# Performance work log

Measured on AMD Instinct MI355X. Metric: run time of the kernel, lower is better.

The kernel has to match this reference:

```python
import jax, jax.numpy as jnp
import numpy as np

B, S = 512, 256
NUM_LOC, NUM_USERS, D = 50000, 10000, 256
MAX_RECENT = 5
DQ = D // 4            # user/hour/weekday embed dim
TEMP = 3 * DQ          # temporal feature size
H2 = D // 2            # scorer hidden
NEG = -1e9


def setup_inputs() -> dict:
    key = jax.random.key(0)
    ks = jax.random.split(key, 25)
    p = lambda i, shape: jax.random.normal(ks[i], shape, jnp.float32) * 0.02

    locations = jax.random.randint(ks[0], (B, S), 0, NUM_LOC)
    users = jax.random.randint(ks[1], (B, S), 0, NUM_USERS)
    weekdays = jax.random.randint(ks[2], (B, S), 0, 8)
    start_mins = jax.random.randint(ks[3], (B, S), 0, 1440)
    lengths = jax.random.randint(ks[4], (B,), 1, S + 1)  # ragged valid lengths
    mask = jnp.arange(S)[None, :] < lengths[:, None]     # (B,S) bool prefix mask

    return {
        "locations": locations, "users": users, "weekdays": weekdays,
        "start_mins": start_mins, "mask": mask,
        # embedding tables (padding_idx=0 row zeroed, matching torch init)
        "loc_table": p(5, (NUM_LOC, D)).at[0].set(0.0),
        "user_table": p(6, (NUM_USERS, DQ)).at[0].set(0.0),
        "hour_table": p(7, (25, DQ)).at[0].set(0.0),
        "wd_table": p(8, (8, DQ)).at[0].set(0.0),
        # LSTM (PyTorch layout: gates i,f,g,o stacked)
        "W_ih": p(9, (4 * D, D + TEMP)), "W_hh": p(10, (4 * D, D)),
        "b_ih": p(11, (4 * D,)), "b_hh": p(12, (4 * D,)),
        # recent-location scorer MLP
        "sc_W1": p(13, (H2, D + 2)), "sc_b1": p(14, (H2,)),
        "sc_W2": p(15, (1, H2)), "sc_b2": p(16, (1,)),
        # new-location predictor MLP (dropout is identity in eval)
        "np_W1": p(17, (D, D)), "np_b1": p(18, (D,)),
        "np_W2": p(19, (NUM_LOC, D)), "np_b2": p(20, (NUM_LOC,)),
        # mix predictor
        "mx_W": p(21, (1, D)), "mx_b": p(22, (1,)),
    }


def _forward(locations, users, weekdays, start_mins, mask,
             loc_table, user_table, hour_table, wd_table,
             W_ih, W_hh, b_ih, b_hh,
             sc_W1, sc_b1, sc_W2, sc_b2,
             np_W1, np_b1, np_W2, np_b2, mx_W, mx_b):
    gelu = lambda x: jax.nn.gelu(x, approximate=False)  # torch nn.GELU default

    hours = jnp.clip(start_mins // 60, 0, 24)
    temporal = jnp.concatenate(
        [user_table[users], hour_table[hours], wd_table[weekdays]], axis=-1)
    x = jnp.concatenate([loc_table[locations], temporal], axis=-1)  # (B,S,D+TEMP)

    # --- LSTM over time via scan (PyTorch gate order i,f,g,o) ---
    def step(carry, xt):
        h, c = carry
        g = xt @ W_ih.T + b_ih + h @ W_hh.T + b_hh
        i, f, gg, o = jnp.split(g, 4, axis=-1)
        c = jax.nn.sigmoid(f) * c + jax.nn.sigmoid(i) * jnp.tanh(gg)
        h = jax.nn.sigmoid(o) * jnp.tanh(c)
        return (h, c), h

    h0 = jnp.zeros((x.shape[0], D), x.dtype)
    _, outs = jax.lax.scan(step, (h0, h0), jnp.swapaxes(x, 0, 1))
    output = jnp.swapaxes(outs, 0, 1)  # (B,S,D)

    seq_lens = mask.sum(axis=1).astype(jnp.int32) - 1  # last valid index
    bids = jnp.arange(output.shape[0])
    context = output[bids, seq_lens]                   # (B,D)

    # --- vectorized ragged recent-location scoring (j=0 is last visit) ---
    j = jnp.arange(MAX_RECENT)
    idx = seq_lens[:, None] - j[None, :]               # (B,R) indices from end
    valid = idx >= 0                                   # j < seq_len_b
    idxc = jnp.clip(idx, 0, S - 1)
    bidx = bids[:, None]
    rlocs = locations[bidx, idxc]                      # (B,R)
    rtimes = start_mins[bidx, idxc]
    cur_time = start_mins[bids, seq_lens][:, None]
    tdiff = ((cur_time - rtimes).astype(jnp.float32) / 1440.0)[..., None]
    pos = jnp.broadcast_to(j.astype(jnp.float32), rlocs.shape)[..., None]
    feats = jnp.concatenate([loc_table[rlocs], tdiff, pos], axis=-1)  # (B,R,D+2)
    scores = (gelu(feats @ sc_W1.T + sc_b1) @ sc_W2.T + sc_b2)[..., 0]  # (B,R)

    # drop entry jj if some newer valid entry j' < jj has the same location.
    eq = rlocs[:, :, None] == rlocs[:, None, :]        # (B, jj, j')
    newer = (j[:, None] > j[None, :])[None]            # jj > j'
    dup = jnp.any(eq & newer & valid[:, None, :], axis=-1)
    keep = valid & ~dup
    scatter_locs = jnp.where(keep, rlocs, NUM_LOC)     # out-of-range -> dropped

    recent_logits = jnp.full((rlocs.shape[0], NUM_LOC), NEG, jnp.float32)
    recent_logits = recent_logits.at[bidx, scatter_locs].set(scores, mode='drop')

    new_logits = gelu(context @ np_W1.T + np_b1) @ np_W2.T + np_b2  # (B,NUM_LOC)
    mix = jax.nn.sigmoid(context @ mx_W.T + mx_b) * 0.9 + 0.05     # (B,1)
    return mix * recent_logits + (1.0 - mix) * new_logits


def reference(locations, users, weekdays, start_mins, mask,
              loc_table, user_table, hour_table, wd_table,
              W_ih, W_hh, b_ih, b_hh,
              sc_W1, sc_b1, sc_W2, sc_b2,
              np_W1, np_b1, np_W2, np_b2, mx_W, mx_b):
    return _forward(locations, users, weekdays, start_mins, mask,
                    loc_table, user_table, hour_table, wd_table,
                    W_ih, W_hh, b_ih, b_hh,
                    sc_W1, sc_b1, sc_W2, sc_b2,
                    np_W1, np_b1, np_W2, np_b2, mx_W, mx_b)
```

## Files before the change

### kernel.cpp

```cpp
#include <hip/hip_runtime.h>
#include <hip/hip_bf16.h>
#include <math.h>

#define B_ 512
#define S_ 256
#define D_ 256
#define NLOC 50000
#define KX 448
#define G4 1024
#define NEGV -1000000000.0f

typedef __attribute__((ext_vector_type(8))) short short8;
typedef __attribute__((ext_vector_type(4))) float f32x4;

__device__ __forceinline__ float sigmoidf_(float x){ return 1.0f/(1.0f+expf(-x)); }
__device__ __forceinline__ float geluf_(float x){ return 0.5f*x*(1.0f+erff(x*0.70710678118654752f)); }
__device__ __forceinline__ unsigned short f2bf_(float x){
  __hip_bfloat16 h = __float2bfloat16(x);
  return *(unsigned short*)&h;
}
__device__ __forceinline__ float bf2f_(unsigned short u){
  __hip_bfloat16 h = *(__hip_bfloat16*)&u;
  return __bfloat162float(h);
}

__global__ void k_init(unsigned short* hbf, float* c, int* flag){
  int i = blockIdx.x*256 + threadIdx.x;
  if (i < B_*D_){ hbf[i]=0; c[i]=0.f; }
  if (i==0) *flag = 0;
}

__global__ void k_detect(const unsigned char* m, int* flag){
  int i = blockIdx.x*256 + threadIdx.x;
  if ((i & 1) && i < B_*S_ && m[i]) atomicOr(flag, 1);
}

__global__ void k_seqlen(const void* mp, const int* flag, int* slens){
  int b = blockIdx.x*256 + threadIdx.x;
  if (b >= B_) return;
  int cnt = 0;
  if (*flag){
    const unsigned char* m = (const unsigned char*)mp;
    for (int s=0;s<S_;s++) cnt += (m[b*S_+s] != 0);
  } else {
    const int* m = (const int*)mp;
    for (int s=0;s<S_;s++) cnt += (m[b*S_+s] != 0);
  }
  slens[b] = cnt - 1;
}

__global__ void k_buildw(const float* wih, const float* whh, const float* bih,
                         const float* bhh, unsigned short* Wihbf,
                         unsigned short* Whhbf, float* btot){
  int i = blockIdx.x*256 + threadIdx.x;
  if (i < G4*KX) Wihbf[i] = f2bf_(wih[i]);
  if (i < G4*D_) Whhbf[i] = f2bf_(whh[i]);
  if (i < G4) btot[i] = bih[i] + bhh[i];
}

__global__ __launch_bounds__(256) void k_gx(
    const int* __restrict__ loc, const int* __restrict__ usr,
    const int* __restrict__ wdy, const int* __restrict__ sm,
    const float* __restrict__ loct, const float* __restrict__ usert,
    const float* __restrict__ hourt, const float* __restrict__ wdt,
    const unsigned short* __restrict__ Wihbf, const float* __restrict__ btot,
    unsigned short* __restrict__ Gx){
  __shared__ unsigned short As[128][40];
  int tid = threadIdx.x;
  int n0 = blockIdx.x*128, m0 = blockIdx.y*128;
  int w = tid>>6, lane = tid&63;
  int quad = lane>>4, l16 = lane&15;
  int mw = (w>>1)*64, nw = (w&1)*64;
  f32x4 acc[4][4] = {};
  int r0 = tid>>2, seg = tid&3;
  for (int kt=0; kt<14; kt++){
    int k0 = kt*32;
    int kc = k0 + seg*8;
    #pragma unroll
    for (int rr=0; rr<2; rr++){
      int r = r0 + rr*64;
      int row = m0 + r;
      const float* src;
      if (kc < 256)      src = loct  + (size_t)loc[row]*256 + kc;
      else if (kc < 320) src = usert + (size_t)usr[row]*64 + (kc-256);
      else if (kc < 384) { int s = sm[row]; int hh = s/60; if (hh>24) hh=24; if (hh<0) hh=0;
                           src = hourt + (size_t)hh*64 + (kc-320); }
      else               src = wdt   + (size_t)wdy[row]*64 + (kc-384);
      float4 v0 = *(const float4*)(src);
      float4 v1 = *(const float4*)(src+4);
      short8 pk;
      pk[0]=f2bf_(v0.x); pk[1]=f2bf_(v0.y); pk[2]=f2bf_(v0.z); pk[3]=f2bf_(v0.w);
      pk[4]=f2bf_(v1.x); pk[5]=f2bf_(v1.y); pk[6]=f2bf_(v1.z); pk[7]=f2bf_(v1.w);
      *(short8*)&As[r][seg*8] = pk;
    }
    __syncthreads();
    short8 bfrag[4], afrag[4];
    #pragma unroll
    for (int nt=0; nt<4; nt++)
      bfrag[nt] = *(const short8*)(Wihbf + (size_t)(n0+nw+nt*16+l16)*KX + k0 + quad*8);
    #pragma unroll
    for (int mt=0; mt<4; mt++)
      afrag[mt] = *(const short8*)&As[mw+mt*16+l16][quad*8];
    #pragma unroll
    for (int mt=0; mt<4; mt++)
      #pragma unroll
      for (int nt=0; nt<4; nt++)
        acc[mt][nt] = __builtin_amdgcn_mfma_f32_16x16x32_bf16(afrag[mt], bfrag[nt], acc[mt][nt], 0, 0, 0);
    __syncthreads();
  }
  #pragma unroll
  for (int nt=0; nt<4; nt++){
    int col = n0 + nw + nt*16 + l16;
    float bv = btot[col];
    #pragma unroll
    for (int mt=0; mt<4; mt++){
      #pragma unroll
      for (int i=0; i<4; i++){
        int row = m0 + mw + mt*16 + quad*4 + i;
        Gx[(size_t)row*G4 + col] = f2bf_(acc[mt][nt][i] + bv);
      }
    }
  }
}

__global__ __launch_bounds__(256) void k_step(int t,
    const unsigned short* __restrict__ Gx, const unsigned short* __restrict__ Whhbf,
    const unsigned short* __restrict__ hin, unsigned short* __restrict__ hout,
    float* __restrict__ c, float* __restrict__ ctx, const int* __restrict__ slens){
  int tid = threadIdx.x;
  int w = tid>>6, lane = tid&63;
  int quad = lane>>4, l16 = lane&15;
  int m0 = blockIdx.x*16;
  int d0 = (blockIdx.y*4 + w)*16;
  f32x4 acc[4] = {};
  #pragma unroll
  for (int kt=0; kt<8; kt++){
    int k0 = kt*32;
    short8 af = *(const short8*)(hin + (size_t)(m0+l16)*D_ + k0 + quad*8);
    #pragma unroll
    for (int q=0; q<4; q++){
      short8 bf = *(const short8*)(Whhbf + (size_t)(q*D_ + d0 + l16)*D_ + k0 + quad*8);
      acc[q] = __builtin_amdgcn_mfma_f32_16x16x32_bf16(af, bf, acc[q], 0, 0, 0);
    }
  }
  int d = d0 + l16;
  #pragma unroll
  for (int i=0; i<4; i++){
    int b = m0 + quad*4 + i;
    size_t gbase = ((size_t)b*S_ + t)*G4;
    float gi = acc[0][i] + bf2f_(Gx[gbase + d]);
    float gf = acc[1][i] + bf2f_(Gx[gbase + 256 + d]);
    float gg = acc[2][i] + bf2f_(Gx[gbase + 512 + d]);
    float go = acc[3][i] + bf2f_(Gx[gbase + 768 + d]);
    size_t ci = (size_t)b*D_ + d;
    float cold = c[ci];
    float cn = sigmoidf_(gf)*cold + sigmoidf_(gi)*tanhf(gg);
    float hn = sigmoidf_(go)*tanhf(cn);
    c[ci] = cn;
    hout[ci] = f2bf_(hn);
    if (t == slens[b]) ctx[ci] = hn;
  }
}

__global__ void k_post1(const float* __restrict__ ctx, const float* __restrict__ W1,
                        const float* __restrict__ b1, const float* __restrict__ mxW,
                        const float* __restrict__ mxb, float* newhid, float* mixv){
  __shared__ float cs[256];
  __shared__ float red[256];
  int b = blockIdx.x, tid = threadIdx.x;
  cs[tid] = ctx[(size_t)b*D_ + tid];
  __syncthreads();
  float a = b1[tid];
  const float* wr = W1 + (size_t)tid*D_;
  for (int k=0; k<D_; k++) a += cs[k]*wr[k];
  newhid[(size_t)b*D_ + tid] = geluf_(a);
  red[tid] = cs[tid]*mxW[tid];
  __syncthreads();
  for (int s=128; s>0; s>>=1){ if (tid<s) red[tid]+=red[tid+s]; __syncthreads(); }
  if (tid==0) mixv[b] = sigmoidf_(red[0]+mxb[0])*0.9f + 0.05f;
}

__global__ void k_recent(const int* __restrict__ loc, const int* __restrict__ sm,
                         const int* __restrict__ slens, const float* __restrict__ loct,
                         const float* __restrict__ W1, const float* __restrict__ b1,
                         const float* __restrict__ W2, const float* __restrict__ b2,
                         float* scores, int* rlocs, int* keep){
  __shared__ int rl[5], vs[5];
  __shared__ float td[5];
  __shared__ float red[128];
  int b = blockIdx.x, tid = threadIdx.x;
  int sl = slens[b];
  if (tid < 5){
    int idx = sl - tid;
    int v = idx >= 0;
    int ic = v ? idx : 0;
    rl[tid] = loc[b*S_ + ic];
    vs[tid] = v;
    int cur = sm[b*S_ + sl];
    td[tid] = (float)(cur - sm[b*S_ + ic]) * (1.0f/1440.0f);
  }
  __syncthreads();
  for (int j=0; j<5; j++){
    const float* lrow = loct + (size_t)rl[j]*D_;
    const float* wr = W1 + (size_t)tid*258;
    float a = b1[tid];
    for (int k=0; k<D_; k++) a += lrow[k]*wr[k];
    a += td[j]*wr[256] + (float)j*wr[257];
    red[tid] = geluf_(a)*W2[tid];
    __syncthreads();
    for (int s=64; s>0; s>>=1){ if (tid<s) red[tid]+=red[tid+s]; __syncthreads(); }
    if (tid==0) scores[b*5+j] = red[0] + b2[0];
    __syncthreads();
  }
  if (tid==0){
    for (int j=0; j<5; j++){
      int dup = 0;
      for (int k=0; k<j; k++) dup |= (rl[j]==rl[k]) && vs[k];
      keep[b*5+j] = vs[j] && !dup;
      rlocs[b*5+j] = rl[j];
    }
  }
}

__global__ __launch_bounds__(256) void k_final(const float* __restrict__ newhid,
    const float* __restrict__ W2, const float* __restrict__ b2,
    const float* __restrict__ mixv, float* __restrict__ out){
  __shared__ float Hs[16][256];
  __shared__ float Wl[64][65];
  int tid = threadIdx.x;
  int l0 = blockIdx.x*64, b0 = blockIdx.y*16;
  int ll = tid & 63, bq = tid >> 6;
  #pragma unroll
  for (int r=0; r<16; r++) Hs[r][tid] = newhid[(size_t)(b0+r)*D_ + tid];
  float acc[4] = {0.f,0.f,0.f,0.f};
  for (int kt=0; kt<4; kt++){
    int k0 = kt*64;
    __syncthreads();
    #pragma unroll
    for (int r=0; r<4; r++){
      int row = 4*r + bq;
      int l = l0 + row;
      Wl[row][ll] = (l < NLOC) ? W2[(size_t)l*D_ + k0 + ll] : 0.f;
    }
    __syncthreads();
    #pragma unroll
    for (int kk=0; kk<64; kk++){
      float wv = Wl[ll][kk];
      #pragma unroll
      for (int bi=0; bi<4; bi++) acc[bi] += wv * Hs[bq*4+bi][k0+kk];
    }
  }
  int l = l0 + ll;
  if (l < NLOC){
    float bias = b2[l];
    #pragma unroll
    for (int bi=0; bi<4; bi++){
      int b = b0 + bq*4 + bi;
      float mx = mixv[b];
      out[(size_t)b*NLOC + l] = mx*NEGV + (1.0f-mx)*(acc[bi] + bias);
    }
  }
}

__global__ void k_scatter(const float* __restrict__ newhid, const float* __restrict__ W2,
                          const float* __restrict__ b2, const float* __restrict__ mixv,
                          const float* __restrict__ scores, const int* __restrict__ rlocs,
                          const int* __restrict__ keep, float* out){
  int b = blockIdx.x, lane = threadIdx.x;
  float mx = mixv[b];
  for (int j=0; j<5; j++){
    if (!keep[b*5+j]) continue;
    int rl = rlocs[b*5+j];
    const float* wr = W2 + (size_t)rl*D_;
    const float* hr = newhid + (size_t)b*D_;
    float a = 0.f;
    #pragma unroll
    for (int q=0; q<4; q++){ int k = lane + 64*q; a += hr[k]*wr[k]; }
    #pragma unroll
    for (int off=32; off>0; off>>=1) a += __shfl_xor(a, off, 64);
    if (lane==0)
      out[(size_t)b*NLOC + rl] = mx*scores[b*5+j] + (1.0f-mx)*(a + b2[rl]);
  }
}

extern "C" void kernel_launch(void* const* d_in, const int* in_sizes, int n_in,
                              void* d_out, int out_size, void* d_ws, size_t ws_size,
                              hipStream_t stream){
  const int* locations   = (const int*)d_in[0];
  const int* users       = (const int*)d_in[1];
  const int* weekdays    = (const int*)d_in[2];
  const int* start_mins  = (const int*)d_in[3];
  const void* mask       = d_in[4];
  const float* loc_table = (const float*)d_in[5];
  const float* user_table= (const float*)d_in[6];
  const float* hour_table= (const float*)d_in[7];
  const float* wd_table  = (const float*)d_in[8];
  const float* W_ih      = (const float*)d_in[9];
  const float* W_hh      = (const float*)d_in[10];
  const float* b_ih      = (const float*)d_in[11];
  const float* b_hh      = (const float*)d_in[12];
  const float* sc_W1     = (const float*)d_in[13];
  const float* sc_b1     = (const float*)d_in[14];
  const float* sc_W2     = (const float*)d_in[15];
  const float* sc_b2     = (const float*)d_in[16];
  const float* np_W1     = (const float*)d_in[17];
  const float* np_b1     = (const float*)d_in[18];
  const float* np_W2     = (const float*)d_in[19];
  const float* np_b2     = (const float*)d_in[20];
  const float* mx_W      = (const float*)d_in[21];
  const float* mx_b      = (const float*)d_in[22];
  float* out = (float*)d_out;

  char* w = (char*)d_ws;
  size_t o = 0;
  auto alloc = [&](size_t bytes)->void*{ void* p = w + o; o += (bytes + 255) & ~(size_t)255; return p; };
  unsigned short* Gx    = (unsigned short*)alloc((size_t)B_*S_*G4*sizeof(short));
  unsigned short* Wihbf = (unsigned short*)alloc((size_t)G4*KX*sizeof(short));
  unsigned short* Whhbf = (unsigned short*)alloc((size_t)G4*D_*sizeof(short));
  float* btot   = (float*)alloc((size_t)G4*sizeof(float));
  unsigned short* hbf0 = (unsigned short*)alloc((size_t)B_*D_*sizeof(short));
  unsigned short* hbf1 = (unsigned short*)alloc((size_t)B_*D_*sizeof(short));
  float* cbuf   = (float*)alloc((size_t)B_*D_*sizeof(float));
  float* ctx    = (float*)alloc((size_t)B_*D_*sizeof(float));
  float* newhid = (float*)alloc((size_t)B_*D_*sizeof(float));
  float* mixv   = (float*)alloc((size_t)B_*sizeof(float));
  float* scores = (float*)alloc((size_t)B_*5*sizeof(float));
  int*   slens  = (int*)alloc((size_t)B_*sizeof(int));
  int*   rlocs  = (int*)alloc((size_t)B_*5*sizeof(int));
  int*   keep   = (int*)alloc((size_t)B_*5*sizeof(int));
  int*   flag   = (int*)alloc(sizeof(int));

  k_init<<<512, 256, 0, stream>>>(hbf0, cbuf, flag);
  k_detect<<<512, 256, 0, stream>>>((const unsigned char*)mask, flag);
  k_seqlen<<<2, 256, 0, stream>>>(mask, flag, slens);
  k_buildw<<<1792, 256, 0, stream>>>(W_ih, W_hh, b_ih, b_hh, Wihbf, Whhbf, btot);
  k_gx<<<dim3(8,1024), 256, 0, stream>>>(locations, users, weekdays, start_mins,
                                         loc_table, user_table, hour_table, wd_table,
                                         Wihbf, btot, Gx);
  for (int t=0; t<S_; t++){
    unsigned short* hin  = (t & 1) ? hbf1 : hbf0;
    unsigned short* hout = (t & 1) ? hbf0 : hbf1;
    k_step<<<dim3(32,4), 256, 0, stream>>>(t, Gx, Whhbf, hin, hout, cbuf, ctx, slens);
  }
  k_post1<<<512, 256, 0, stream>>>(ctx, np_W1, np_b1, mx_W, mx_b, newhid, mixv);
  k_recent<<<512, 128, 0, stream>>>(locations, start_mins, slens, loc_table,
                                    sc_W1, sc_b1, sc_W2, sc_b2, scores, rlocs, keep);
  k_final<<<dim3(782,32), 256, 0, stream>>>(newhid, np_W2, np_b2, mixv, out);
  k_scatter<<<512, 64, 0, stream>>>(newhid, np_W2, np_b2, mixv, scores, rlocs, keep, out);
}
```

Before: 3.580 ms.

## Fuse LSTM timesteps into one persistent kernel with grid-wide flag barrier

Replaces 256 per-timestep launches with a single persistent kernel of 128 blocks. Each block keeps its W_hh slice in LDS and the cell state in registers, and prefetches the next step's Gx. Gx is re-laid out time-major so the prefetch reads contiguous rows. Blocks synchronise each step through atomic flags with release/acquire spinning, which removes launch overhead and repeated weight loads. This relies on all 128 blocks being co-resident, or the spin barrier will deadlock.

```diff
diff --git a/kernel.cpp b/kernel.cpp
--- a/kernel.cpp
+++ b/kernel.cpp
@@ -9,6 +9,7 @@
 #define KX 448
 #define G4 1024
 #define NEGV -1000000000.0f
+#define NBLK 128
 
 typedef __attribute__((ext_vector_type(8))) short short8;
 typedef __attribute__((ext_vector_type(4))) float f32x4;
@@ -24,9 +25,10 @@
   return __bfloat162float(h);
 }
 
-__global__ void k_init(unsigned short* hbf, float* c, int* flag){
+__global__ void k_init(unsigned short* hbf, int* flags, int* flag){
   int i = blockIdx.x*256 + threadIdx.x;
-  if (i < B_*D_){ hbf[i]=0; c[i]=0.f; }
+  if (i < B_*D_) hbf[i]=0;
+  if (i < NBLK*16) flags[i]=0;
   if (i==0) *flag = 0;
 }
 
@@ -117,48 +119,98 @@
       #pragma unroll
       for (int i=0; i<4; i++){
         int row = m0 + mw + mt*16 + quad*4 + i;
-        Gx[(size_t)row*G4 + col] = f2bf_(acc[mt][nt][i] + bv);
+        int b = row >> 8, t = row & 255;
+        Gx[((size_t)t*B_ + b)*G4 + col] = f2bf_(acc[mt][nt][i] + bv);
       }
     }
   }
 }
 
-__global__ __launch_bounds__(256) void k_step(int t,
+__global__ __launch_bounds__(256,1) void k_lstm_all(
     const unsigned short* __restrict__ Gx, const unsigned short* __restrict__ Whhbf,
-    const unsigned short* __restrict__ hin, unsigned short* __restrict__ hout,
-    float* __restrict__ c, float* __restrict__ ctx, const int* __restrict__ slens){
+    unsigned short* __restrict__ hbf0, unsigned short* __restrict__ hbf1,
+    float* __restrict__ ctx, const int* __restrict__ slens, int* flags){
+  __shared__ unsigned short WsF[32768];
   int tid = threadIdx.x;
+  int bx = blockIdx.x;
+  int b0 = (bx >> 3) * 32;
+  int d0 = (bx & 7) * 32;
   int w = tid>>6, lane = tid&63;
   int quad = lane>>4, l16 = lane&15;
-  int m0 = blockIdx.x*16;
-  int d0 = (blockIdx.y*4 + w)*16;
-  f32x4 acc[4] = {};
-  #pragma unroll
-  for (int kt=0; kt<8; kt++){
-    int k0 = kt*32;
-    short8 af = *(const short8*)(hin + (size_t)(m0+l16)*D_ + k0 + quad*8);
-    #pragma unroll
-    for (int q=0; q<4; q++){
-      short8 bf = *(const short8*)(Whhbf + (size_t)(q*D_ + d0 + l16)*D_ + k0 + quad*8);
-      acc[q] = __builtin_amdgcn_mfma_f32_16x16x32_bf16(af, bf, acc[q], 0, 0, 0);
-    }
-  }
-  int d = d0 + l16;
-  #pragma unroll
-  for (int i=0; i<4; i++){
-    int b = m0 + quad*4 + i;
-    size_t gbase = ((size_t)b*S_ + t)*G4;
-    float gi = acc[0][i] + bf2f_(Gx[gbase + d]);
-    float gf = acc[1][i] + bf2f_(Gx[gbase + 256 + d]);
-    float gg = acc[2][i] + bf2f_(Gx[gbase + 512 + d]);
-    float go = acc[3][i] + bf2f_(Gx[gbase + 768 + d]);
-    size_t ci = (size_t)b*D_ + d;
-    float cold = c[ci];
-    float cn = sigmoidf_(gf)*cold + sigmoidf_(gi)*tanhf(gg);
-    float hn = sigmoidf_(go)*tanhf(cn);
-    c[ci] = cn;
-    hout[ci] = f2bf_(hn);
-    if (t == slens[b]) ctx[ci] = hn;
+  int dwi = w & 1, mw = (w>>1)*16;
+
+  #pragma unroll
+  for (int j=0; j<16; j++){
+    int f = tid + 256*j;
+    int fl = f & 63;
+    int fdwi = (f>>6)&1, fq = (f>>7)&3, fkt = f>>9;
+    int grow = fq*256 + d0 + fdwi*16 + (fl&15);
+    int gk = fkt*32 + (fl>>4)*8;
+    *(short8*)&WsF[f*8] = *(const short8*)(Whhbf + (size_t)grow*D_ + gk);
+  }
+  __syncthreads();
+
+  f32x4 creg = {0.f,0.f,0.f,0.f};
+  int d = d0 + dwi*16 + l16;
+  int brow[4], sl[4];
+  #pragma unroll
+  for (int i=0;i<4;i++){ brow[i] = b0 + mw + quad*4 + i; sl[i] = slens[brow[i]]; }
+
+  unsigned short gxr[4][4];
+  #pragma unroll
+  for (int q=0;q<4;q++)
+    #pragma unroll
+    for (int i=0;i<4;i++)
+      gxr[q][i] = Gx[((size_t)0*B_ + brow[i])*G4 + q*256 + d];
+
+  for (int t=0; t<S_; t++){
+    const unsigned short* hi = (t & 1) ? hbf1 : hbf0;
+    unsigned short*       ho = (t & 1) ? hbf0 : hbf1;
+    f32x4 acc[4] = {};
+    #pragma unroll
+    for (int kt=0; kt<8; kt++){
+      short8 af = *(const short8*)(hi + (size_t)(b0+mw+l16)*D_ + kt*32 + quad*8);
+      #pragma unroll
+      for (int q=0; q<4; q++){
+        short8 bf = *(const short8*)&WsF[((((kt*4+q)*2)+dwi)*64 + lane)*8];
+        acc[q] = __builtin_amdgcn_mfma_f32_16x16x32_bf16(af, bf, acc[q], 0, 0, 0);
+      }
+    }
+    #pragma unroll
+    for (int i=0; i<4; i++){
+      int b = brow[i];
+      float gi = acc[0][i] + bf2f_(gxr[0][i]);
+      float gf = acc[1][i] + bf2f_(gxr[1][i]);
+      float gg = acc[2][i] + bf2f_(gxr[2][i]);
+      float go = acc[3][i] + bf2f_(gxr[3][i]);
+      float cn = sigmoidf_(gf)*creg[i] + sigmoidf_(gi)*tanhf(gg);
+      float hn = sigmoidf_(go)*tanhf(cn);
+      creg[i] = cn;
+      ho[(size_t)b*D_ + d] = f2bf_(hn);
+      if (t == sl[i]) ctx[(size_t)b*D_ + d] = hn;
+    }
+    if (t < S_-1){
+      #pragma unroll
+      for (int q=0;q<4;q++)
+        #pragma unroll
+        for (int i=0;i<4;i++)
+          gxr[q][i] = Gx[((size_t)(t+1)*B_ + brow[i])*G4 + q*256 + d];
+      __syncthreads();
+      if (tid == 0){
+        __threadfence();
+        __hip_atomic_store(&flags[bx*16], t+1, __ATOMIC_RELEASE, __HIP_MEMORY_SCOPE_AGENT);
+      }
+      if (tid < 64){
+        int tp1 = t+1;
+        for(;;){
+          int f0 = __hip_atomic_load(&flags[tid*16],      __ATOMIC_ACQUIRE, __HIP_MEMORY_SCOPE_AGENT);
+          int f1 = __hip_atomic_load(&flags[(tid+64)*16], __ATOMIC_ACQUIRE, __HIP_MEMORY_SCOPE_AGENT);
+          if (__all(f0 >= tp1 && f1 >= tp1)) break;
+          __builtin_amdgcn_s_sleep(1);
+        }
+      }
+      __syncthreads();
+    }
   }
 }
 
@@ -320,7 +372,6 @@
   float* btot   = (float*)alloc((size_t)G4*sizeof(float));
   unsigned short* hbf0 = (unsigned short*)alloc((size_t)B_*D_*sizeof(short));
   unsigned short* hbf1 = (unsigned short*)alloc((size_t)B_*D_*sizeof(short));
-  float* cbuf   = (float*)alloc((size_t)B_*D_*sizeof(float));
   float* ctx    = (float*)alloc((size_t)B_*D_*sizeof(float));
   float* newhid = (float*)alloc((size_t)B_*D_*sizeof(float));
   float* mixv   = (float*)alloc((size_t)B_*sizeof(float));
@@ -328,20 +379,17 @@
   int*   slens  = (int*)alloc((size_t)B_*sizeof(int));
   int*   rlocs  = (int*)alloc((size_t)B_*5*sizeof(int));
   int*   keep   = (int*)alloc((size_t)B_*5*sizeof(int));
+  int*   flags  = (int*)alloc((size_t)NBLK*16*sizeof(int));
   int*   flag   = (int*)alloc(sizeof(int));
 
-  k_init<<<512, 256, 0, stream>>>(hbf0, cbuf, flag);
+  k_init<<<512, 256, 0, stream>>>(hbf0, flags, flag);
   k_detect<<<512, 256, 0, stream>>>((const unsigned char*)mask, flag);
   k_seqlen<<<2, 256, 0, stream>>>(mask, flag, slens);
   k_buildw<<<1792, 256, 0, stream>>>(W_ih, W_hh, b_ih, b_hh, Wihbf, Whhbf, btot);
   k_gx<<<dim3(8,1024), 256, 0, stream>>>(locations, users, weekdays, start_mins,
                                          loc_table, user_table, hour_table, wd_table,
                                          Wihbf, btot, Gx);
-  for (int t=0; t<S_; t++){
-    unsigned short* hin  = (t & 1) ? hbf1 : hbf0;
-    unsigned short* hout = (t & 1) ? hbf0 : hbf1;
-    k_step<<<dim3(32,4), 256, 0, stream>>>(t, Gx, Whhbf, hin, hout, cbuf, ctx, slens);
-  }
+  k_lstm_all<<<NBLK, 256, 0, stream>>>(Gx, Whhbf, hbf0, hbf1, ctx, slens, flags);
   k_post1<<<512, 256, 0, stream>>>(ctx, np_W1, np_b1, mx_W, mx_b, newhid, mixv);
   k_recent<<<512, 128, 0, stream>>>(locations, start_mins, slens, loc_table,
                                     sc_W1, sc_b1, sc_W2, sc_b2, scores, rlocs, keep);
```

New measurement: 4.680 ms. 1.31x slower.

## Fuse LSTM time loop into one persistent kernel with time-major Gx

Applied to the files above, without the earlier changes.

Replaces the 256 per-timestep k_step launches with a single kernel of 32 blocks. Each block owns 16 batch rows and loops over all timesteps, keeping the cell state in registers and syncing only within the block, since its rows do not depend on other blocks. Gx is rewritten in time-major order so each step reads a contiguous slab. This removes launch overhead and the global round-trips for c. The cost is much less parallelism (32 blocks instead of 128), and each block streams all of W_hh from cache on every step.

```diff
diff --git a/kernel.cpp b/kernel.cpp
--- a/kernel.cpp
+++ b/kernel.cpp
@@ -117,48 +117,74 @@
       #pragma unroll
       for (int i=0; i<4; i++){
         int row = m0 + mw + mt*16 + quad*4 + i;
-        Gx[(size_t)row*G4 + col] = f2bf_(acc[mt][nt][i] + bv);
+        int b = row >> 8, t = row & 255;
+        Gx[((size_t)t*B_ + b)*G4 + col] = f2bf_(acc[mt][nt][i] + bv);
       }
     }
   }
 }
 
-__global__ __launch_bounds__(256) void k_step(int t,
+__global__ __launch_bounds__(256,1) void k_lstm_seq(
     const unsigned short* __restrict__ Gx, const unsigned short* __restrict__ Whhbf,
-    const unsigned short* __restrict__ hin, unsigned short* __restrict__ hout,
-    float* __restrict__ c, float* __restrict__ ctx, const int* __restrict__ slens){
+    unsigned short* __restrict__ h0, unsigned short* __restrict__ h1,
+    float* __restrict__ cbuf, float* __restrict__ ctx, const int* __restrict__ slens){
   int tid = threadIdx.x;
   int w = tid>>6, lane = tid&63;
   int quad = lane>>4, l16 = lane&15;
-  int m0 = blockIdx.x*16;
-  int d0 = (blockIdx.y*4 + w)*16;
-  f32x4 acc[4] = {};
+  int b0 = blockIdx.x*16;
+
+  int brow[4], sl[4];
   #pragma unroll
-  for (int kt=0; kt<8; kt++){
-    int k0 = kt*32;
-    short8 af = *(const short8*)(hin + (size_t)(m0+l16)*D_ + k0 + quad*8);
-    #pragma unroll
-    for (int q=0; q<4; q++){
-      short8 bf = *(const short8*)(Whhbf + (size_t)(q*D_ + d0 + l16)*D_ + k0 + quad*8);
-      acc[q] = __builtin_amdgcn_mfma_f32_16x16x32_bf16(af, bf, acc[q], 0, 0, 0);
-    }
-  }
-  int d = d0 + l16;
+  for (int i=0;i<4;i++){ brow[i] = b0 + quad*4 + i; sl[i] = slens[brow[i]]; }
+
+  float cst[4][4];
   #pragma unroll
-  for (int i=0; i<4; i++){
-    int b = m0 + quad*4 + i;
-    size_t gbase = ((size_t)b*S_ + t)*G4;
-    float gi = acc[0][i] + bf2f_(Gx[gbase + d]);
-    float gf = acc[1][i] + bf2f_(Gx[gbase + 256 + d]);
-    float gg = acc[2][i] + bf2f_(Gx[gbase + 512 + d]);
-    float go = acc[3][i] + bf2f_(Gx[gbase + 768 + d]);
-    size_t ci = (size_t)b*D_ + d;
-    float cold = c[ci];
-    float cn = sigmoidf_(gf)*cold + sigmoidf_(gi)*tanhf(gg);
-    float hn = sigmoidf_(go)*tanhf(cn);
-    c[ci] = cn;
-    hout[ci] = f2bf_(hn);
-    if (t == slens[b]) ctx[ci] = hn;
+  for (int j=0;j<4;j++)
+    #pragma unroll
+    for (int i=0;i<4;i++)
+      cst[j][i] = cbuf[(size_t)brow[i]*D_ + w*64 + j*16 + l16];
+
+  for (int t=0; t<S_; t++){
+    const unsigned short* hin = (t & 1) ? h1 : h0;
+    unsigned short*       hout= (t & 1) ? h0 : h1;
+    short8 af[8];
+    #pragma unroll
+    for (int kt=0; kt<8; kt++)
+      af[kt] = *(const short8*)(hin + (size_t)(b0+l16)*D_ + kt*32 + quad*8);
+    f32x4 acc[4][4] = {};
+    #pragma unroll
+    for (int j=0; j<4; j++){
+      int dj = w*64 + j*16;
+      #pragma unroll
+      for (int q=0; q<4; q++){
+        const unsigned short* wp = Whhbf + (size_t)(q*256 + dj + l16)*D_ + quad*8;
+        #pragma unroll
+        for (int kt=0; kt<8; kt++){
+          short8 bf = *(const short8*)(wp + kt*32);
+          acc[j][q] = __builtin_amdgcn_mfma_f32_16x16x32_bf16(af[kt], bf, acc[j][q], 0, 0, 0);
+        }
+      }
+    }
+    #pragma unroll
+    for (int j=0; j<4; j++){
+      int d = w*64 + j*16 + l16;
+      #pragma unroll
+      for (int i=0; i<4; i++){
+        int b = brow[i];
+        size_t gbase = ((size_t)t*B_ + b)*G4;
+        float gi = acc[j][0][i] + bf2f_(Gx[gbase +        d]);
+        float gf = acc[j][1][i] + bf2f_(Gx[gbase + 256  + d]);
+        float gg = acc[j][2][i] + bf2f_(Gx[gbase + 512  + d]);
+        float go = acc[j][3][i] + bf2f_(Gx[gbase + 768  + d]);
+        float cn = sigmoidf_(gf)*cst[j][i] + sigmoidf_(gi)*tanhf(gg);
+        float hn = sigmoidf_(go)*tanhf(cn);
+        cst[j][i] = cn;
+        hout[(size_t)b*D_ + d] = f2bf_(hn);
+        if (t == sl[i]) ctx[(size_t)b*D_ + d] = hn;
+      }
+    }
+    __threadfence();
+    __syncthreads();
   }
 }
 
@@ -337,11 +363,7 @@
   k_gx<<<dim3(8,1024), 256, 0, stream>>>(locations, users, weekdays, start_mins,
                                          loc_table, user_table, hour_table, wd_table,
                                          Wihbf, btot, Gx);
-  for (int t=0; t<S_; t++){
-    unsigned short* hin  = (t & 1) ? hbf1 : hbf0;
-    unsigned short* hout = (t & 1) ? hbf0 : hbf1;
-    k_step<<<dim3(32,4), 256, 0, stream>>>(t, Gx, Whhbf, hin, hout, cbuf, ctx, slens);
-  }
+  k_lstm_seq<<<32, 256, 0, stream>>>(Gx, Whhbf, hbf0, hbf1, cbuf, ctx, slens);
   k_post1<<<512, 256, 0, stream>>>(ctx, np_W1, np_b1, mx_W, mx_b, newhid, mixv);
   k_recent<<<512, 128, 0, stream>>>(locations, start_mins, slens, loc_table,
                                     sc_W1, sc_b1, sc_W2, sc_b2, scores, rlocs, keep);
```

After: 5.585 ms. 56.0% more time.
